# Performance work log

Measured on AMD Instinct MI355X. Metric: run time of the kernel, lower is better.

## Reference

```python
import jax, jax.numpy as jnp
import numpy as np

C = 256
HEADS = 8
HEAD_DIM = C // HEADS
GROUPS = 8
EPS = 1e-5


def setup_inputs() -> dict:
    key = jax.random.key(0)
    ks = jax.random.split(key, 11)
    B, S = 2, 16
    s = 0.02
    return {
        "x": jax.random.normal(ks[0], (B, C, S, S, S), dtype=jnp.float32),
        "gn_w": jnp.ones((C,), jnp.float32),
        "gn_b": jnp.zeros((C,), jnp.float32),
        "wq": jax.random.normal(ks[1], (C, C), jnp.float32) * s,
        "bq": jnp.zeros((C,), jnp.float32),
        "wk": jax.random.normal(ks[2], (C, C), jnp.float32) * s,
        "bk": jnp.zeros((C,), jnp.float32),
        "wv": jax.random.normal(ks[3], (C, C), jnp.float32) * s,
        "bv": jnp.zeros((C,), jnp.float32),
        "wo": jax.random.normal(ks[4], (C, C), jnp.float32) * s,
        "bo": jnp.zeros((C,), jnp.float32),
    }


def _group_norm(x, w, b):
    # x: [B, C, D, H, W]; GroupNorm(8, C) with affine params
    B, Cc, D, H, W = x.shape
    xg = x.reshape(B, GROUPS, Cc // GROUPS, D, H, W)
    mu = jnp.mean(xg, axis=(2, 3, 4, 5), keepdims=True)
    var = jnp.mean(jnp.square(xg - mu), axis=(2, 3, 4, 5), keepdims=True)
    xn = ((xg - mu) * jax.lax.rsqrt(var + EPS)).reshape(B, Cc, D, H, W)
    return xn * w[None, :, None, None, None] + b[None, :, None, None, None]


def reference(x, gn_w, gn_b, wq, bq, wk, bk, wv, bv, wo, bo):
    B, Cc, D, H, W = x.shape
    N = D * H * W
    xn = _group_norm(x, gn_w, gn_b).reshape(B, Cc, N)  # [B,C,N]
    # 1x1x1 Conv3d == per-voxel linear: weight [out,in]
    Q = jnp.einsum("oc,bcn->bon", wq, xn) + bq[None, :, None]
    K = jnp.einsum("oc,bcn->bon", wk, xn) + bk[None, :, None]
    V = jnp.einsum("oc,bcn->bon", wv, xn) + bv[None, :, None]
    Q = Q.reshape(B, HEADS, HEAD_DIM, N)
    K = K.reshape(B, HEADS, HEAD_DIM, N)
    V = V.reshape(B, HEADS, HEAD_DIM, N)
    scale = np.sqrt(HEAD_DIM).astype(np.float32)
    attn = jnp.einsum("bhdn,bhdm->bhnm", Q, K) / scale
    attn = jax.nn.softmax(attn, axis=-1)
    out = jnp.einsum("bhnm,bhdm->bhdn", attn, V)  # [B,h,hd,N]
    out = out.reshape(B, Cc, N)
    out = jnp.einsum("oc,bcn->bon", wo, out) + bo[None, :, None]
    return x + out.reshape(B, Cc, D, H, W)
```

## Files before the change

### kernel.cpp

```cpp
#include <hip/hip_runtime.h>

#define B_   2
#define C_   256
#define N_   4096
#define H_   8
#define HD_  32
#define G_   8
#define CPG_ 32

typedef short short8 __attribute__((ext_vector_type(8)));
typedef short short4v __attribute__((ext_vector_type(4)));
typedef unsigned uint4v __attribute__((ext_vector_type(4)));
typedef float f32x4  __attribute__((ext_vector_type(4)));
typedef float f4     __attribute__((ext_vector_type(4)));

__device__ __forceinline__ float b2f(short s) {
    return __uint_as_float(((unsigned)(unsigned short)s) << 16);
}
__device__ __forceinline__ short f2b(float f) {
    unsigned u = __float_as_uint(f);
    unsigned r = (u + 0x7FFF + ((u >> 16) & 1)) >> 16;
    return (short)r;
}

__global__ __launch_bounds__(256) void gn_part(const float* __restrict__ x,
                                               float* __restrict__ part) {
    int blk = blockIdx.x;
    const f4* p = (const f4*)x + (size_t)(blk >> 6) * (CPG_ * N_ / 4) + (size_t)(blk & 63) * 512;
    float s = 0.f, ss = 0.f;
#pragma unroll
    for (int i = 0; i < 2; i++) {
        f4 v = p[threadIdx.x + i * 256];
#pragma unroll
        for (int j = 0; j < 4; j++) { float f = v[j]; s += f; ss += f * f; }
    }
#pragma unroll
    for (int off = 32; off > 0; off >>= 1) {
        s  += __shfl_down(s, off);
        ss += __shfl_down(ss, off);
    }
    __shared__ float rs[4], rss[4];
    int w = threadIdx.x >> 6;
    if ((threadIdx.x & 63) == 0) { rs[w] = s; rss[w] = ss; }
    __syncthreads();
    if (threadIdx.x == 0) {
        part[blk * 2]     = rs[0] + rs[1] + rs[2] + rs[3];
        part[blk * 2 + 1] = rss[0] + rss[1] + rss[2] + rss[3];
    }
}

__global__ __launch_bounds__(256) void gemm_qkv(
    const float* __restrict__ x,
    const float* __restrict__ gw, const float* __restrict__ gb,
    const float* __restrict__ part,
    const float* __restrict__ wq, const float* __restrict__ bq,
    const float* __restrict__ wk, const float* __restrict__ bk,
    const float* __restrict__ wv, const float* __restrict__ bv,
    short* __restrict__ q, short* __restrict__ kt, short* __restrict__ v) {
    int z = blockIdx.z;
    int b = z / 3, which = z % 3;
    const float* W    = which == 0 ? wq : (which == 1 ? wk : wv);
    const float* bias = which == 0 ? bq : (which == 1 ? bk : bv);
    bool trans = (which != 2);
    float mul = (which == 0) ? (0.17677669529663687f * 1.4426950408889634f) : 1.0f;

    __shared__ short wl[64][40];
    __shared__ short xl[128][40];
    __shared__ float ga[256], gbb[256];
    __shared__ float mus[8], rstds[8];

    int o0 = blockIdx.y * 64, n0 = blockIdx.x * 128;
    int tid = threadIdx.x;
    int w = tid >> 6, lane = tid & 63, li = lane & 15, quad = lane >> 4;
    int wr = w & 1, wc = w >> 1;

#pragma unroll
    for (int gi = 0; gi < 2; gi++) {
        int g = w * 2 + gi;
        const float* pp = &part[(size_t)(b * 8 + g) * 128 + lane * 2];
        float s = pp[0], ss = pp[1];
#pragma unroll
        for (int off = 32; off > 0; off >>= 1) {
            s  += __shfl_down(s, off);
            ss += __shfl_down(ss, off);
        }
        if (lane == 0) {
            const float inv = 1.f / (float)(CPG_ * N_);
            float mu = s * inv;
            float var = ss * inv - mu * mu;
            mus[g] = mu;
            rstds[g] = rsqrtf(var + 1e-5f);
        }
    }
    __syncthreads();
    {
        int c = tid, g = c >> 5;
        float a = rstds[g] * gw[c];
        ga[c]  = a;
        gbb[c] = gb[c] - mus[g] * a;
    }

    f32x4 acc[8];
#pragma unroll
    for (int i = 0; i < 8; i++) acc[i] = (f32x4){0.f, 0.f, 0.f, 0.f};

    int cpair = tid >> 4, l16 = tid & 15;
    __syncthreads();

    for (int k0 = 0; k0 < 256; k0 += 32) {
        {
            int row = tid >> 2, co = (tid & 3) << 3;
            const float* wp = &W[(size_t)(o0 + row) * 256 + k0 + co];
            f4 wa = *(const f4*)wp;
            f4 wb = *(const f4*)(wp + 4);
            short8 w8;
#pragma unroll
            for (int j = 0; j < 4; j++) { w8[j] = f2b(wa[j]); w8[j + 4] = f2b(wb[j]); }
            *(short8*)&wl[row][co] = w8;
        }
        {
            int c0 = k0 + cpair * 2;
            float a0 = ga[c0],     b0c = gbb[c0];
            float a1 = ga[c0 + 1], b1c = gbb[c0 + 1];
            const float* xr0 = x + ((size_t)(b * 256 + c0)) * N_ + n0 + l16;
            const float* xr1 = xr0 + N_;
#pragma unroll
            for (int j = 0; j < 8; j++) {
                unsigned lo = (unsigned short)f2b(xr0[16 * j] * a0 + b0c);
                unsigned hi = (unsigned short)f2b(xr1[16 * j] * a1 + b1c);
                *(unsigned*)&xl[l16 + 16 * j][cpair * 2] = lo | (hi << 16);
            }
        }
        __syncthreads();
        short8 af[4], bfr[4];
        if (trans) {
#pragma unroll
            for (int i = 0; i < 4; i++) af[i]  = *(short8*)&xl[wr * 64 + i * 16 + li][quad * 8];
#pragma unroll
            for (int j = 0; j < 2; j++) bfr[j] = *(short8*)&wl[wc * 32 + j * 16 + li][quad * 8];
#pragma unroll
            for (int i = 0; i < 4; i++)
#pragma unroll
                for (int j = 0; j < 2; j++)
                    acc[i * 2 + j] = __builtin_amdgcn_mfma_f32_16x16x32_bf16(af[i], bfr[j], acc[i * 2 + j], 0, 0, 0);
        } else {
#pragma unroll
            for (int i = 0; i < 2; i++) af[i]  = *(short8*)&wl[wr * 32 + i * 16 + li][quad * 8];
#pragma unroll
            for (int j = 0; j < 4; j++) bfr[j] = *(short8*)&xl[wc * 64 + j * 16 + li][quad * 8];
#pragma unroll
            for (int i = 0; i < 2; i++)
#pragma unroll
                for (int j = 0; j < 4; j++)
                    acc[i * 4 + j] = __builtin_amdgcn_mfma_f32_16x16x32_bf16(af[i], bfr[j], acc[i * 4 + j], 0, 0, 0);
        }
        __syncthreads();
    }

    if (which == 2) {
        short* outp = v + (size_t)b * C_ * N_;
#pragma unroll
        for (int i = 0; i < 2; i++) {
            int ob = o0 + wr * 32 + i * 16 + quad * 4;
#pragma unroll
            for (int j = 0; j < 4; j++) {
                int n_ = n0 + wc * 64 + j * 16 + li;
#pragma unroll
                for (int r = 0; r < 4; r++) {
                    float val = acc[i * 4 + j][r] + bias[ob + r];
                    outp[(size_t)(ob + r) * N_ + n_] = f2b(val);
                }
            }
        }
    } else if (which == 0) {
        short* outp = q + (size_t)b * N_ * C_;
#pragma unroll
        for (int i = 0; i < 4; i++) {
            int nb_ = n0 + wr * 64 + i * 16 + quad * 4;
#pragma unroll
            for (int j = 0; j < 2; j++) {
                int o_ = o0 + wc * 32 + j * 16 + li;
                float bv_ = bias[o_];
#pragma unroll
                for (int r = 0; r < 4; r++)
                    outp[(size_t)(nb_ + r) * C_ + o_] = f2b((acc[i * 2 + j][r] + bv_) * mul);
            }
        }
    } else {
#pragma unroll
        for (int i = 0; i < 4; i++) {
            int nb_ = n0 + wr * 64 + i * 16 + quad * 4;
#pragma unroll
            for (int j = 0; j < 2; j++) {
                int o_ = o0 + wc * 32 + j * 16 + li;
                int hh = o_ >> 5, d = o_ & 31;
                float bv_ = bias[o_];
                short* kdst = kt + ((size_t)(b * 8 + hh) * N_) * HD_ + d;
#pragma unroll
                for (int r = 0; r < 4; r++)
                    kdst[(size_t)(nb_ + r) * HD_] = f2b(acc[i * 2 + j][r] + bv_);
            }
        }
    }
}

__global__ __launch_bounds__(512) void flash(const short* __restrict__ q,
                                             const short* __restrict__ ktp,
                                             const short* __restrict__ v,
                                             float* __restrict__ Opart,
                                             float* __restrict__ lrbuf,
                                             int nsplit, int nt) {
    int bid = blockIdx.x;
    int xcd = bid & 7;
    int rest = bid >> 3;
    int bh = xcd * 2 + (rest & 1);
    int r2 = rest >> 1;
    int nb = r2 & 15;
    int qt = r2 >> 4;
    int b = bh >> 3, h = bh & 7;
    int moff = qt * (N_ / 4) * (nsplit == 2 ? 2 : 1);

    const short* QT = q   + (size_t)b * N_ * C_ + h * HD_;
    const short* KP = ktp + (size_t)bh * N_ * HD_ + (size_t)moff * HD_;
    const short* V  = v   + ((size_t)b * C_ + h * HD_) * N_ + moff;
    const size_t TS = (size_t)B_ * N_ * C_;
    float* Oh  = Opart + (size_t)qt * TS + (size_t)b * N_ * C_ + h * HD_;
    float* lrp = lrbuf + ((size_t)qt * 16 + bh) * N_;

    __shared__ short kl[2 * 2560];
    __shared__ short vl[2 * 2304];

    int tid = threadIdx.x, w = tid >> 6, lane = tid & 63, li = lane & 15, quad = lane >> 4;
    int n0w = nb * 256 + w * 32;

    short8 qf0 = *(const short8*)&QT[(size_t)(n0w + li) * 256 + quad * 8];
    short8 qf1 = *(const short8*)&QT[(size_t)(n0w + 16 + li) * 256 + quad * 8];

    f32x4 oa00 = (f32x4){0.f,0.f,0.f,0.f}, oa01 = oa00, oa10 = oa00, oa11 = oa00;
    float lr0 = 0.f, lr1 = 0.f;
    const f32x4 zero = (f32x4){0.f, 0.f, 0.f, 0.f};

    int krow = tid >> 3, kcol = (tid & 7) << 2;
    const short* kgp = KP + (size_t)krow * HD_ + kcol;
    int klo = krow * 40 + kcol;
    int vd = tid >> 4, g = tid & 15;
    int mbase = 32 * (g >> 3) + 16 * (g & 1) + 4 * ((g >> 1) & 3);
    const short* vgp = V + (size_t)vd * N_ + mbase;
    int vlo = vd * 72 + g * 4;

    short4v kst = *(const short4v*)kgp;
    short4v vst = *(const short4v*)vgp;

    f32x4 s0[4], s1[4];
    short8 vf[4];

    for (int t = 0; t < nt; ++t) {
        int buf = t & 1;
        *(short4v*)&kl[buf * 2560 + klo] = kst;
        *(short4v*)&vl[buf * 2304 + vlo] = vst;
        if (t < nt - 1) {
            kst = *(const short4v*)(kgp + (size_t)(t + 1) * 64 * HD_);
            vst = *(const short4v*)(vgp + (t + 1) * 64);
        }
        __syncthreads();

        __builtin_amdgcn_s_setprio(1);
#pragma unroll
        for (int c = 0; c < 4; c++) {
            short8 kf = *(short8*)&kl[buf * 2560 + (c * 16 + li) * 40 + quad * 8];
            s0[c] = __builtin_amdgcn_mfma_f32_16x16x32_bf16(kf, qf0, zero, 0, 0, 0);
            s1[c] = __builtin_amdgcn_mfma_f32_16x16x32_bf16(kf, qf1, zero, 0, 0, 0);
        }
        __builtin_amdgcn_s_setprio(0);

        vf[0] = *(short8*)&vl[buf * 2304 + li * 72 + quad * 8];
        vf[1] = *(short8*)&vl[buf * 2304 + (16 + li) * 72 + quad * 8];
        vf[2] = *(short8*)&vl[buf * 2304 + li * 72 + 32 + quad * 8];
        vf[3] = *(short8*)&vl[buf * 2304 + (16 + li) * 72 + 32 + quad * 8];

        unsigned paw[8];
        float lp = 0.f;
#pragma unroll
        for (int c = 0; c < 4; c++) {
            float e0 = __builtin_amdgcn_exp2f(s0[c][0]);
            float e1 = __builtin_amdgcn_exp2f(s0[c][1]);
            float e2 = __builtin_amdgcn_exp2f(s0[c][2]);
            float e3 = __builtin_amdgcn_exp2f(s0[c][3]);
            lp += (e0 + e1) + (e2 + e3);
            paw[2 * c]     = __builtin_amdgcn_perm(__float_as_uint(e1), __float_as_uint(e0), 0x07060302);
            paw[2 * c + 1] = __builtin_amdgcn_perm(__float_as_uint(e3), __float_as_uint(e2), 0x07060302);
        }
        lr0 += lp;
        uint4v p0 = (uint4v){paw[0], paw[1], paw[2], paw[3]};
        uint4v p1 = (uint4v){paw[4], paw[5], paw[6], paw[7]};
        short8 a0 = __builtin_bit_cast(short8, p0);
        short8 a1 = __builtin_bit_cast(short8, p1);

        lp = 0.f;
#pragma unroll
        for (int c = 0; c < 4; c++) {
            float e0 = __builtin_amdgcn_exp2f(s1[c][0]);
            float e1 = __builtin_amdgcn_exp2f(s1[c][1]);
            float e2 = __builtin_amdgcn_exp2f(s1[c][2]);
            float e3 = __builtin_amdgcn_exp2f(s1[c][3]);
            lp += (e0 + e1) + (e2 + e3);
            paw[2 * c]     = __builtin_amdgcn_perm(__float_as_uint(e1), __float_as_uint(e0), 0x07060302);
            paw[2 * c + 1] = __builtin_amdgcn_perm(__float_as_uint(e3), __float_as_uint(e2), 0x07060302);
        }
        lr1 += lp;
        uint4v p2 = (uint4v){paw[0], paw[1], paw[2], paw[3]};
        uint4v p3 = (uint4v){paw[4], paw[5], paw[6], paw[7]};
        short8 a2 = __builtin_bit_cast(short8, p2);
        short8 a3 = __builtin_bit_cast(short8, p3);

        __builtin_amdgcn_s_setprio(1);
        oa00 = __builtin_amdgcn_mfma_f32_16x16x32_bf16(a0, vf[0], oa00, 0, 0, 0);
        oa01 = __builtin_amdgcn_mfma_f32_16x16x32_bf16(a0, vf[1], oa01, 0, 0, 0);
        oa00 = __builtin_amdgcn_mfma_f32_16x16x32_bf16(a1, vf[2], oa00, 0, 0, 0);
        oa01 = __builtin_amdgcn_mfma_f32_16x16x32_bf16(a1, vf[3], oa01, 0, 0, 0);
        oa10 = __builtin_amdgcn_mfma_f32_16x16x32_bf16(a2, vf[0], oa10, 0, 0, 0);
        oa11 = __builtin_amdgcn_mfma_f32_16x16x32_bf16(a2, vf[1], oa11, 0, 0, 0);
        oa10 = __builtin_amdgcn_mfma_f32_16x16x32_bf16(a3, vf[2], oa10, 0, 0, 0);
        oa11 = __builtin_amdgcn_mfma_f32_16x16x32_bf16(a3, vf[3], oa11, 0, 0, 0);
        __builtin_amdgcn_s_setprio(0);
    }

    lr0 += __shfl_xor(lr0, 16); lr0 += __shfl_xor(lr0, 32);
    lr1 += __shfl_xor(lr1, 16); lr1 += __shfl_xor(lr1, 32);
#pragma unroll
    for (int r = 0; r < 4; r++) {
        size_t n_ = (size_t)(n0w + quad * 4 + r);
        Oh[n_ * 256 + li]      = oa00[r];
        Oh[n_ * 256 + 16 + li] = oa01[r];
        size_t n2 = (size_t)(n0w + 16 + quad * 4 + r);
        Oh[n2 * 256 + li]      = oa10[r];
        Oh[n2 * 256 + 16 + li] = oa11[r];
    }
    if (quad == 0) {
        lrp[n0w + li]      = lr0;
        lrp[n0w + 16 + li] = lr1;
    }
}

__global__ __launch_bounds__(256) void combine(const float* __restrict__ Opart,
                                               const float* __restrict__ lrbuf,
                                               short* __restrict__ aoT,
                                               int nsplit) {
    int idx = blockIdx.x * 256 + threadIdx.x;
    int cg = idx & 31;
    int n  = (idx >> 5) & 4095;
    int b  = idx >> 17;
    int c0 = cg * 8;
    int bh = b * 8 + (c0 >> 5);
    const size_t TS = (size_t)B_ * N_ * C_;
    float l = 0.f;
    for (int qt = 0; qt < nsplit; ++qt)
        l += lrbuf[((size_t)qt * 16 + bh) * N_ + n];
    float inv = 1.f / l;
    size_t base = ((size_t)b * N_ + n) * 256 + c0;
    f4 a0 = (f4){0.f,0.f,0.f,0.f}, a1 = a0;
    for (int qt = 0; qt < nsplit; ++qt) {
        const float* p = Opart + (size_t)qt * TS + base;
        a0 += *(const f4*)p;
        a1 += *(const f4*)(p + 4);
    }
    short8 r;
#pragma unroll
    for (int j = 0; j < 4; j++) {
        r[j]     = f2b(a0[j] * inv);
        r[j + 4] = f2b(a1[j] * inv);
    }
    *(short8*)&aoT[base] = r;
}

__global__ __launch_bounds__(256) void gemm_out(const float* __restrict__ W,
                                                const float* __restrict__ bias,
                                                const short* __restrict__ aoT,
                                                const float* __restrict__ resid,
                                                float* __restrict__ out) {
    int b = blockIdx.z;
    const short* X = aoT + (size_t)b * N_ * C_;
    const float* R = resid + (size_t)b * C_ * N_;
    float* outp = out + (size_t)b * C_ * N_;

    __shared__ short wl[128][40];
    __shared__ short xl[64][40];

    int o0 = blockIdx.y * 128, n0 = blockIdx.x * 64;
    int tid = threadIdx.x;
    int w = tid >> 6, lane = tid & 63, li = lane & 15, quad = lane >> 4;
    int wr = w & 1, wc = w >> 1;

    f32x4 acc[4][2];
#pragma unroll
    for (int i = 0; i < 4; i++)
#pragma unroll
        for (int j = 0; j < 2; j++) acc[i][j] = (f32x4){0.f, 0.f, 0.f, 0.f};

    for (int k0 = 0; k0 < 256; k0 += 32) {
#pragma unroll
        for (int i = 0; i < 2; i++) {
            int idx = tid + i * 256;
            int row = idx >> 2, co = (idx & 3) << 3;
            const float* wp = &W[(size_t)(o0 + row) * 256 + k0 + co];
            f4 wa = *(const f4*)wp;
            f4 wb = *(const f4*)(wp + 4);
            short8 w8;
#pragma unroll
            for (int j = 0; j < 4; j++) { w8[j] = f2b(wa[j]); w8[j + 4] = f2b(wb[j]); }
            *(short8*)&wl[row][co] = w8;
        }
        {
            int row = tid >> 2, co = (tid & 3) << 3;
            *(short8*)&xl[row][co] = *(const short8*)&X[(size_t)(n0 + row) * 256 + k0 + co];
        }
        __syncthreads();
        short8 af[4], bfr[2];
#pragma unroll
        for (int i = 0; i < 4; i++) af[i]  = *(short8*)&wl[wr * 64 + i * 16 + li][quad * 8];
#pragma unroll
        for (int j = 0; j < 2; j++) bfr[j] = *(short8*)&xl[wc * 32 + j * 16 + li][quad * 8];
#pragma unroll
        for (int i = 0; i < 4; i++)
#pragma unroll
            for (int j = 0; j < 2; j++)
                acc[i][j] = __builtin_amdgcn_mfma_f32_16x16x32_bf16(af[i], bfr[j], acc[i][j], 0, 0, 0);
        __syncthreads();
    }
#pragma unroll
    for (int i = 0; i < 4; i++) {
        int ob = o0 + wr * 64 + i * 16 + quad * 4;
#pragma unroll
        for (int j = 0; j < 2; j++) {
            int n_ = n0 + wc * 32 + j * 16 + li;
#pragma unroll
            for (int r = 0; r < 4; r++) {
                size_t idx = (size_t)(ob + r) * N_ + n_;
                outp[idx] = acc[i][j][r] + bias[ob + r] + R[idx];
            }
        }
    }
}

extern "C" void kernel_launch(void* const* d_in, const int* in_sizes, int n_in,
                              void* d_out, int out_size, void* d_ws, size_t ws_size,
                              hipStream_t stream) {
    const float* x  = (const float*)d_in[0];
    const float* gw = (const float*)d_in[1];
    const float* gb = (const float*)d_in[2];
    const float* wq = (const float*)d_in[3];
    const float* bq = (const float*)d_in[4];
    const float* wk = (const float*)d_in[5];
    const float* bk = (const float*)d_in[6];
    const float* wv = (const float*)d_in[7];
    const float* bv = (const float*)d_in[8];
    const float* wo = (const float*)d_in[9];
    const float* bo = (const float*)d_in[10];
    float* out = (float*)d_out;

    char* ws = (char*)d_ws;
    float* part = (float*)ws;
    const size_t TS = (size_t)B_ * N_ * C_;
    short* aoT = (short*)(ws + 16384);
    short* q   = aoT + TS;
    short* kt  = q + TS;
    short* v   = kt + TS;
    float* Of  = (float*)(v + TS);
    int SP = (ws_size >= (size_t)52 * 1024 * 1024) ? 4 : 2;
    float* lr  = Of + (size_t)SP * TS;

    gn_part<<<1024, 256, 0, stream>>>(x, part);
    gemm_qkv<<<dim3(32, 4, 6), 256, 0, stream>>>(x, gw, gb, part,
                                                 wq, bq, wk, bk, wv, bv, q, kt, v);
    flash<<<SP * 256, 512, 0, stream>>>(q, kt, v, Of, lr, SP, 64 / SP);
    combine<<<1024, 256, 0, stream>>>(Of, lr, aoT, SP);
    gemm_out<<<dim3(64, 2, 2), 256, 0, stream>>>(wo, bo, aoT, x, out);
}
```

Before: 155.1 us.

## Give each flash wave 64 query rows and halve the block to 256 threads

The flash kernel now launches 256-thread blocks in which each of 4 waves handles 64 query rows instead of 32. Each wave reads the K and V fragments from LDS once and reuses them across four query sub-tiles. The global-to-LDS staging is remapped so each thread moves 8 elements of K and V, and the exp/pack code is factored into a macro. The aim is to cut LDS reads and barrier cost per unit of MFMA work. In exchange each wave holds more accumulator registers, and the block has fewer waves to hide latency, with launch bounds set for 3 blocks per CU.

```diff
diff --git a/kernel.cpp b/kernel.cpp
--- a/kernel.cpp
+++ b/kernel.cpp
@@ -204,12 +204,33 @@
     }
 }
 
-__global__ __launch_bounds__(512) void flash(const short* __restrict__ q,
-                                             const short* __restrict__ ktp,
-                                             const short* __restrict__ v,
-                                             float* __restrict__ Opart,
-                                             float* __restrict__ lrbuf,
-                                             int nsplit, int nt) {
+#define EXPPACK(sx, lrx, A0, A1)                                          \
+    {                                                                     \
+        unsigned paw[8];                                                  \
+        float lp = 0.f;                                                   \
+        _Pragma("unroll")                                                 \
+        for (int c = 0; c < 4; c++) {                                     \
+            float e0 = __builtin_amdgcn_exp2f(sx[c][0]);                  \
+            float e1 = __builtin_amdgcn_exp2f(sx[c][1]);                  \
+            float e2 = __builtin_amdgcn_exp2f(sx[c][2]);                  \
+            float e3 = __builtin_amdgcn_exp2f(sx[c][3]);                  \
+            lp += (e0 + e1) + (e2 + e3);                                  \
+            paw[2 * c]     = __builtin_amdgcn_perm(__float_as_uint(e1), __float_as_uint(e0), 0x07060302); \
+            paw[2 * c + 1] = __builtin_amdgcn_perm(__float_as_uint(e3), __float_as_uint(e2), 0x07060302); \
+        }                                                                 \
+        lrx += lp;                                                        \
+        uint4v p0_ = (uint4v){paw[0], paw[1], paw[2], paw[3]};            \
+        uint4v p1_ = (uint4v){paw[4], paw[5], paw[6], paw[7]};            \
+        A0 = __builtin_bit_cast(short8, p0_);                             \
+        A1 = __builtin_bit_cast(short8, p1_);                             \
+    }
+
+__global__ __launch_bounds__(256, 3) void flash(const short* __restrict__ q,
+                                                const short* __restrict__ ktp,
+                                                const short* __restrict__ v,
+                                                float* __restrict__ Opart,
+                                                float* __restrict__ lrbuf,
+                                                int nsplit, int nt) {
     int bid = blockIdx.x;
     int xcd = bid & 7;
     int rest = bid >> 3;
@@ -218,7 +239,7 @@
     int nb = r2 & 15;
     int qt = r2 >> 4;
     int b = bh >> 3, h = bh & 7;
-    int moff = qt * (N_ / 4) * (nsplit == 2 ? 2 : 1);
+    int moff = qt * (N_ / nsplit);
 
     const short* QT = q   + (size_t)b * N_ * C_ + h * HD_;
     const short* KP = ktp + (size_t)bh * N_ * HD_ + (size_t)moff * HD_;
@@ -231,45 +252,55 @@
     __shared__ short vl[2 * 2304];
 
     int tid = threadIdx.x, w = tid >> 6, lane = tid & 63, li = lane & 15, quad = lane >> 4;
-    int n0w = nb * 256 + w * 32;
+    int n0w = nb * 256 + w * 64;
 
     short8 qf0 = *(const short8*)&QT[(size_t)(n0w + li) * 256 + quad * 8];
     short8 qf1 = *(const short8*)&QT[(size_t)(n0w + 16 + li) * 256 + quad * 8];
+    short8 qf2 = *(const short8*)&QT[(size_t)(n0w + 32 + li) * 256 + quad * 8];
+    short8 qf3 = *(const short8*)&QT[(size_t)(n0w + 48 + li) * 256 + quad * 8];
 
     f32x4 oa00 = (f32x4){0.f,0.f,0.f,0.f}, oa01 = oa00, oa10 = oa00, oa11 = oa00;
-    float lr0 = 0.f, lr1 = 0.f;
+    f32x4 oa20 = oa00, oa21 = oa00, oa30 = oa00, oa31 = oa00;
+    float lr0 = 0.f, lr1 = 0.f, lr2 = 0.f, lr3 = 0.f;
     const f32x4 zero = (f32x4){0.f, 0.f, 0.f, 0.f};
 
-    int krow = tid >> 3, kcol = (tid & 7) << 2;
+    int krow = tid >> 2, kcol = (tid & 3) << 3;
     const short* kgp = KP + (size_t)krow * HD_ + kcol;
     int klo = krow * 40 + kcol;
-    int vd = tid >> 4, g = tid & 15;
-    int mbase = 32 * (g >> 3) + 16 * (g & 1) + 4 * ((g >> 1) & 3);
+    int vd = tid >> 3, g8 = tid & 7;
+    int mbase = 32 * (g8 >> 2) + 4 * (g8 & 3);
     const short* vgp = V + (size_t)vd * N_ + mbase;
-    int vlo = vd * 72 + g * 4;
-
-    short4v kst = *(const short4v*)kgp;
-    short4v vst = *(const short4v*)vgp;
+    int vlo = vd * 72 + g8 * 8;
+
+    short8 kst = *(const short8*)kgp;
+    short4v vstl = *(const short4v*)vgp;
+    short4v vsth = *(const short4v*)(vgp + 16);
 
     f32x4 s0[4], s1[4];
-    short8 vf[4];
+    short8 vf[4], a0, a1, a2, a3;
 
     for (int t = 0; t < nt; ++t) {
         int buf = t & 1;
-        *(short4v*)&kl[buf * 2560 + klo] = kst;
-        *(short4v*)&vl[buf * 2304 + vlo] = vst;
+        *(short8*)&kl[buf * 2560 + klo] = kst;
+        *(short4v*)&vl[buf * 2304 + vlo] = vstl;
+        *(short4v*)&vl[buf * 2304 + vlo + 4] = vsth;
         if (t < nt - 1) {
-            kst = *(const short4v*)(kgp + (size_t)(t + 1) * 64 * HD_);
-            vst = *(const short4v*)(vgp + (t + 1) * 64);
+            kst  = *(const short8*)(kgp + (size_t)(t + 1) * 64 * HD_);
+            vstl = *(const short4v*)(vgp + (t + 1) * 64);
+            vsth = *(const short4v*)(vgp + (t + 1) * 64 + 16);
         }
         __syncthreads();
 
+        short8 kf[4];
+#pragma unroll
+        for (int c = 0; c < 4; c++)
+            kf[c] = *(short8*)&kl[buf * 2560 + (c * 16 + li) * 40 + quad * 8];
+
         __builtin_amdgcn_s_setprio(1);
 #pragma unroll
         for (int c = 0; c < 4; c++) {
-            short8 kf = *(short8*)&kl[buf * 2560 + (c * 16 + li) * 40 + quad * 8];
-            s0[c] = __builtin_amdgcn_mfma_f32_16x16x32_bf16(kf, qf0, zero, 0, 0, 0);
-            s1[c] = __builtin_amdgcn_mfma_f32_16x16x32_bf16(kf, qf1, zero, 0, 0, 0);
+            s0[c] = __builtin_amdgcn_mfma_f32_16x16x32_bf16(kf[c], qf0, zero, 0, 0, 0);
+            s1[c] = __builtin_amdgcn_mfma_f32_16x16x32_bf16(kf[c], qf1, zero, 0, 0, 0);
         }
         __builtin_amdgcn_s_setprio(0);
 
@@ -278,40 +309,8 @@
         vf[2] = *(short8*)&vl[buf * 2304 + li * 72 + 32 + quad * 8];
         vf[3] = *(short8*)&vl[buf * 2304 + (16 + li) * 72 + 32 + quad * 8];
 
-        unsigned paw[8];
-        float lp = 0.f;
-#pragma unroll
-        for (int c = 0; c < 4; c++) {
-            float e0 = __builtin_amdgcn_exp2f(s0[c][0]);
-            float e1 = __builtin_amdgcn_exp2f(s0[c][1]);
-            float e2 = __builtin_amdgcn_exp2f(s0[c][2]);
-            float e3 = __builtin_amdgcn_exp2f(s0[c][3]);
-            lp += (e0 + e1) + (e2 + e3);
-            paw[2 * c]     = __builtin_amdgcn_perm(__float_as_uint(e1), __float_as_uint(e0), 0x07060302);
-            paw[2 * c + 1] = __builtin_amdgcn_perm(__float_as_uint(e3), __float_as_uint(e2), 0x07060302);
-        }
-        lr0 += lp;
-        uint4v p0 = (uint4v){paw[0], paw[1], paw[2], paw[3]};
-        uint4v p1 = (uint4v){paw[4], paw[5], paw[6], paw[7]};
-        short8 a0 = __builtin_bit_cast(short8, p0);
-        short8 a1 = __builtin_bit_cast(short8, p1);
-
-        lp = 0.f;
-#pragma unroll
-        for (int c = 0; c < 4; c++) {
-            float e0 = __builtin_amdgcn_exp2f(s1[c][0]);
-            float e1 = __builtin_amdgcn_exp2f(s1[c][1]);
-            float e2 = __builtin_amdgcn_exp2f(s1[c][2]);
-            float e3 = __builtin_amdgcn_exp2f(s1[c][3]);
-            lp += (e0 + e1) + (e2 + e3);
-            paw[2 * c]     = __builtin_amdgcn_perm(__float_as_uint(e1), __float_as_uint(e0), 0x07060302);
-            paw[2 * c + 1] = __builtin_amdgcn_perm(__float_as_uint(e3), __float_as_uint(e2), 0x07060302);
-        }
-        lr1 += lp;
-        uint4v p2 = (uint4v){paw[0], paw[1], paw[2], paw[3]};
-        uint4v p3 = (uint4v){paw[4], paw[5], paw[6], paw[7]};
-        short8 a2 = __builtin_bit_cast(short8, p2);
-        short8 a3 = __builtin_bit_cast(short8, p3);
+        EXPPACK(s0, lr0, a0, a1);
+        EXPPACK(s1, lr1, a2, a3);
 
         __builtin_amdgcn_s_setprio(1);
         oa00 = __builtin_amdgcn_mfma_f32_16x16x32_bf16(a0, vf[0], oa00, 0, 0, 0);
@@ -323,22 +322,54 @@
         oa10 = __builtin_amdgcn_mfma_f32_16x16x32_bf16(a3, vf[2], oa10, 0, 0, 0);
         oa11 = __builtin_amdgcn_mfma_f32_16x16x32_bf16(a3, vf[3], oa11, 0, 0, 0);
         __builtin_amdgcn_s_setprio(0);
+
+        __builtin_amdgcn_s_setprio(1);
+#pragma unroll
+        for (int c = 0; c < 4; c++) {
+            s0[c] = __builtin_amdgcn_mfma_f32_16x16x32_bf16(kf[c], qf2, zero, 0, 0, 0);
+            s1[c] = __builtin_amdgcn_mfma_f32_16x16x32_bf16(kf[c], qf3, zero, 0, 0, 0);
+        }
+        __builtin_amdgcn_s_setprio(0);
+
+        EXPPACK(s0, lr2, a0, a1);
+        EXPPACK(s1, lr3, a2, a3);
+
+        __builtin_amdgcn_s_setprio(1);
+        oa20 = __builtin_amdgcn_mfma_f32_16x16x32_bf16(a0, vf[0], oa20, 0, 0, 0);
+        oa21 = __builtin_amdgcn_mfma_f32_16x16x32_bf16(a0, vf[1], oa21, 0, 0, 0);
+        oa20 = __builtin_amdgcn_mfma_f32_16x16x32_bf16(a1, vf[2], oa20, 0, 0, 0);
+        oa21 = __builtin_amdgcn_mfma_f32_16x16x32_bf16(a1, vf[3], oa21, 0, 0, 0);
+        oa30 = __builtin_amdgcn_mfma_f32_16x16x32_bf16(a2, vf[0], oa30, 0, 0, 0);
+        oa31 = __builtin_amdgcn_mfma_f32_16x16x32_bf16(a2, vf[1], oa31, 0, 0, 0);
+        oa30 = __builtin_amdgcn_mfma_f32_16x16x32_bf16(a3, vf[2], oa30, 0, 0, 0);
+        oa31 = __builtin_amdgcn_mfma_f32_16x16x32_bf16(a3, vf[3], oa31, 0, 0, 0);
+        __builtin_amdgcn_s_setprio(0);
     }
 
     lr0 += __shfl_xor(lr0, 16); lr0 += __shfl_xor(lr0, 32);
     lr1 += __shfl_xor(lr1, 16); lr1 += __shfl_xor(lr1, 32);
+    lr2 += __shfl_xor(lr2, 16); lr2 += __shfl_xor(lr2, 32);
+    lr3 += __shfl_xor(lr3, 16); lr3 += __shfl_xor(lr3, 32);
 #pragma unroll
     for (int r = 0; r < 4; r++) {
-        size_t n_ = (size_t)(n0w + quad * 4 + r);
-        Oh[n_ * 256 + li]      = oa00[r];
-        Oh[n_ * 256 + 16 + li] = oa01[r];
-        size_t n2 = (size_t)(n0w + 16 + quad * 4 + r);
-        Oh[n2 * 256 + li]      = oa10[r];
-        Oh[n2 * 256 + 16 + li] = oa11[r];
+        size_t n0_ = (size_t)(n0w + quad * 4 + r);
+        Oh[n0_ * 256 + li]      = oa00[r];
+        Oh[n0_ * 256 + 16 + li] = oa01[r];
+        size_t n1_ = (size_t)(n0w + 16 + quad * 4 + r);
+        Oh[n1_ * 256 + li]      = oa10[r];
+        Oh[n1_ * 256 + 16 + li] = oa11[r];
+        size_t n2_ = (size_t)(n0w + 32 + quad * 4 + r);
+        Oh[n2_ * 256 + li]      = oa20[r];
+        Oh[n2_ * 256 + 16 + li] = oa21[r];
+        size_t n3_ = (size_t)(n0w + 48 + quad * 4 + r);
+        Oh[n3_ * 256 + li]      = oa30[r];
+        Oh[n3_ * 256 + 16 + li] = oa31[r];
     }
     if (quad == 0) {
         lrp[n0w + li]      = lr0;
         lrp[n0w + 16 + li] = lr1;
+        lrp[n0w + 32 + li] = lr2;
+        lrp[n0w + 48 + li] = lr3;
     }
 }
 
@@ -472,7 +503,7 @@
     gn_part<<<1024, 256, 0, stream>>>(x, part);
     gemm_qkv<<<dim3(32, 4, 6), 256, 0, stream>>>(x, gw, gb, part,
                                                  wq, bq, wk, bk, wv, bv, q, kt, v);
-    flash<<<SP * 256, 512, 0, stream>>>(q, kt, v, Of, lr, SP, 64 / SP);
+    flash<<<SP * 256, 256, 0, stream>>>(q, kt, v, Of, lr, SP, (N_ / SP) / 64);
     combine<<<1024, 256, 0, stream>>>(Of, lr, aoT, SP);
     gemm_out<<<dim3(64, 2, 2), 256, 0, stream>>>(wo, bo, aoT, x, out);
 }
```

Measured after the change: 164.7 us. +6.1%, slower.
